# Optimization experiments

Hardware: AMD Instinct MI355X
Metric: run time of the kernel (lower is better)

Reference implementation:

```python
import jax, jax.numpy as jnp
import numpy as np

B, N, D, H = 8, 1024, 768, 12
DH = D // H
SCALE = D ** (-0.5)  # standard_scale=False => dim**-0.5


def setup_inputs() -> dict:
    key = jax.random.key(0)
    ks = jax.random.split(key, 6)
    x = jax.random.normal(ks[0], (B, N, D), dtype=jnp.float32)
    gamma = jax.random.uniform(ks[1], (B,), dtype=jnp.float32)
    dist = jax.random.uniform(ks[2], (N, N), dtype=jnp.float32)
    W_qkv = jax.random.normal(ks[3], (D, 3 * D), dtype=jnp.float32) * (D ** -0.5)
    b_qkv = jnp.zeros((3 * D,), dtype=jnp.float32)
    W_proj = jax.random.normal(ks[4], (D, D), dtype=jnp.float32) * (D ** -0.5)
    b_proj = jnp.zeros((D,), dtype=jnp.float32)
    return {"x": x, "gamma": gamma, "dist": dist, "W_qkv": W_qkv,
            "b_qkv": b_qkv, "W_proj": W_proj, "b_proj": b_proj}


def reference(x, gamma, dist, W_qkv, b_qkv, W_proj, b_proj):
    # qkv projection: [B,N,3D] -> [3,B,H,N,DH]
    qkv = (x @ W_qkv + b_qkv).reshape(B, N, 3, H, DH).transpose(2, 0, 3, 1, 4)
    q, k, v = qkv[0], qkv[1], qkv[2]
    # scores [B,H,N,N] with learned per-batch distance bias
    scores = jnp.einsum('bhnd,bhmd->bhnm', q, k) * SCALE
    scores = scores - gamma[:, None, None, None] * dist[None, None, :, :]
    attn = jax.nn.softmax(scores, axis=-1)
    out = jnp.einsum('bhnm,bhmd->bhnd', attn, v)
    out = out.transpose(0, 2, 1, 3).reshape(B, N, D)  # [B,N,D]
    return out @ W_proj + b_proj
```

## Files before the change

### kernel.cpp

```cpp
#include <hip/hip_runtime.h>
#include <hip/hip_bf16.h>
#include <cstdint>
#include <cstddef>

#define B_  8
#define N_  1024
#define D_  768
#define H_  12
#define DH_ 64
#define M_  (B_*N_)
#define D3_ (3*D_)

typedef __bf16 bf16;
typedef __bf16 bf16x4 __attribute__((ext_vector_type(4)));
typedef __bf16 bf16x8 __attribute__((ext_vector_type(8)));
typedef float  floatx4 __attribute__((ext_vector_type(4)));

__device__ __forceinline__ void async16(const void* g, void* l) {
  __builtin_amdgcn_global_load_lds(
      (const __attribute__((address_space(1))) unsigned int*)g,
      (__attribute__((address_space(3))) unsigned int*)l, 16, 0, 0);
}

__global__ __launch_bounds__(256) void detect_small_k(
    const unsigned int* __restrict__ xraw, const void* bq, const void* bp,
    const void* gm, int* __restrict__ flag, bf16* bqd, bf16* bpd, float* gmd) {
  __shared__ int sc;
  if (threadIdx.x == 0) sc = 0;
  __syncthreads();
  int cnt = 0;
  for (int j = 0; j < 8; j++) {
    unsigned int w = xraw[threadIdx.x * 8 + j];
    unsigned int e = (w >> 7) & 0xFF;
    cnt += (e >= 100 && e <= 140) ? 1 : 0;
  }
  atomicAdd(&sc, cnt);
  __syncthreads();
  int f = (sc > 1024) ? 1 : 0;
  if (threadIdx.x == 0) *flag = f;
  for (int i = threadIdx.x; i < D3_; i += 256)
    bqd[i] = f ? ((const bf16*)bq)[i] : (bf16)((const float*)bq)[i];
  for (int i = threadIdx.x; i < D_; i += 256)
    bpd[i] = f ? ((const bf16*)bp)[i] : (bf16)((const float*)bp)[i];
  if (threadIdx.x < B_)
    gmd[threadIdx.x] = f ? (float)((const bf16*)gm)[threadIdx.x]
                         : ((const float*)gm)[threadIdx.x];
}

__device__ __forceinline__ void ingest_span(const void* src, bf16* dst, int f,
                                            long n4, long i0, long stride) {
  if (f) {
    const ushort2* s = (const ushort2*)src;
    ushort2* d = (ushort2*)dst;
    for (long i = i0; i < n4 * 2; i += stride) d[i] = s[i];
  } else {
    const float4* s = (const float4*)src;
    for (long i = i0; i < n4; i += stride) {
      float4 v = s[i];
      bf16x4 o = { (bf16)v.x, (bf16)v.y, (bf16)v.z, (bf16)v.w };
      *(bf16x4*)(dst + i * 4) = o;
    }
  }
}
#define XBLOCKS 1024
#define DBLOCKS 256
__global__ __launch_bounds__(256) void ingest2_k(const void* __restrict__ x,
                                                 bf16* __restrict__ xb,
                                                 const void* __restrict__ dist,
                                                 bf16* __restrict__ distb,
                                                 const int* __restrict__ flag) {
  int f = *flag;
  if (blockIdx.x < XBLOCKS) {
    long i0 = (long)blockIdx.x * 256 + threadIdx.x;
    ingest_span(x, xb, f, (long)M_ * D_ / 4, i0, (long)XBLOCKS * 256);
  } else {
    long i0 = (long)(blockIdx.x - XBLOCKS) * 256 + threadIdx.x;
    ingest_span(dist, distb, f, (long)N_ * N_ / 4, i0, (long)DBLOCKS * 256);
  }
}

__global__ __launch_bounds__(256) void ingest_wt_k(const void* srcA, bf16* dstA,
                                                   const void* srcB, bf16* dstB,
                                                   const int* __restrict__ flag,
                                                   int tilesA, int tcA) {
  __shared__ bf16 t[64][72];
  int f = *flag;
  int bid = blockIdx.x;
  const void* src; bf16* dst; int C;
  int tc;
  if (bid < tilesA) { src = srcA; dst = dstA; C = D3_; tc = tcA; }
  else { bid -= tilesA; src = srcB; dst = dstB; C = D_; tc = D_ / 64; }
  int c0 = (bid % tc) * 64, r0 = (bid / tc) * 64;
  int i = threadIdx.x >> 2, j0 = (threadIdx.x & 3) * 16;
  if (f) {
    const bf16* s = (const bf16*)src + (size_t)(r0 + i) * C + c0 + j0;
#pragma unroll
    for (int jj = 0; jj < 16; jj += 8) *(bf16x8*)&t[i][j0 + jj] = *(const bf16x8*)(s + jj);
  } else {
    const float4* s = (const float4*)((const float*)src + (size_t)(r0 + i) * C + c0 + j0);
#pragma unroll
    for (int jj = 0; jj < 4; jj++) {
      float4 v = s[jj];
      bf16x4 o = { (bf16)v.x, (bf16)v.y, (bf16)v.z, (bf16)v.w };
      *(bf16x4*)&t[i][j0 + jj * 4] = o;
    }
  }
  __syncthreads();
  bf16* d = dst + (size_t)(c0 + i) * D_ + r0 + j0;
#pragma unroll
  for (int jj = 0; jj < 16; jj++) d[jj] = t[j0 + jj][i];
}

template <int MODE, int TMI, int BYL>
__global__ __launch_bounds__(256) void gemm_bt(const bf16* __restrict__ A,
                                               const bf16* __restrict__ Bt,
                                               const bf16* __restrict__ bias,
                                               bf16* __restrict__ O0,
                                               bf16* __restrict__ O1,
                                               bf16* __restrict__ O2,
                                               float* __restrict__ OF,
                                               const int* __restrict__ flag,
                                               int Kdim) {
  constexpr int TM = TMI * 32;
  constexpr int ASZ = 2 * TM * 32;
  int id = blockIdx.x;
  int xcd = id & 7;
  int j = id >> 3;
  int bx = j / BYL;
  int by = xcd * BYL + (j % BYL);
  int n0 = bx * 128, m0 = by * TM;
  int tid = threadIdx.x, wave = tid >> 6, lane = tid & 63;
  int wm = (wave >> 1) * (TMI * 16), wn = (wave & 1) * 64;
  int cl = lane & 15, qd = lane >> 4;
  __shared__ __align__(16) bf16 sh[ASZ + 2 * 128 * 32];
  floatx4 acc[TMI][4] = {};

  int srow = lane >> 2, sko = (lane & 3) * 8;

  auto stage = [&](int kt, int b) {
#pragma unroll
    for (int i = 0; i < TMI / 2; i++) {
      int c = wave * (TMI / 2) + i;
      int row = c * 16 + srow;
      async16(A + (size_t)(m0 + row) * Kdim + kt + sko,
              (char*)sh + (size_t)b * (TM * 64) + c * 1024);
    }
#pragma unroll
    for (int i = 0; i < 2; i++) {
      int c = wave * 2 + i;
      int row = c * 16 + srow;
      async16(Bt + (size_t)(n0 + row) * Kdim + kt + sko,
              (char*)sh + (size_t)ASZ * 2 + (size_t)b * 8192 + c * 1024);
    }
  };
  auto compute = [&](int b) {
    const bf16* Ab = sh + (size_t)b * (TM * 32);
    const bf16* Bb = sh + ASZ + (size_t)b * (128 * 32);
    bf16x8 af[TMI], bfv[4];
#pragma unroll
    for (int mi = 0; mi < TMI; mi++)
      af[mi] = *(const bf16x8*)(Ab + (wm + mi * 16 + cl) * 32 + qd * 8);
#pragma unroll
    for (int ni = 0; ni < 4; ni++)
      bfv[ni] = *(const bf16x8*)(Bb + (wn + ni * 16 + cl) * 32 + qd * 8);
#pragma unroll
    for (int mi = 0; mi < TMI; mi++)
#pragma unroll
      for (int ni = 0; ni < 4; ni++)
        acc[mi][ni] = __builtin_amdgcn_mfma_f32_16x16x32_bf16(af[mi], bfv[ni],
                                                              acc[mi][ni], 0, 0, 0);
  };

  stage(0, 0);
  for (int kt = 0; kt < Kdim; kt += 64) {
    __syncthreads();
    if (kt + 32 < Kdim) stage(kt + 32, 1);
    compute(0);
    __syncthreads();
    if (kt + 64 < Kdim) stage(kt + 64, 0);
    if (kt + 32 < Kdim) compute(1);
  }

  if constexpr (MODE == 0) {
    int t = n0 / D_;
    int h0 = (n0 % D_) >> 6;
    int b = m0 >> 10;
    int nbase = m0 & 1023;
    bf16* Ot = (t == 0) ? O0 : O1;
    __syncthreads();
#pragma unroll
    for (int hh = 0; hh < 2; hh++) {
      if ((wave >> 1) == hh) {
#pragma unroll
        for (int ni = 0; ni < 4; ni++) {
          int col = wn + ni * 16 + cl;
          float bv = (float)bias[n0 + col];
          int s = (col >> 3) & 7;
#pragma unroll
          for (int mi = 0; mi < TMI; mi++) {
            int qpos = (mi * 4 + qd) ^ s;
            bf16x4 w = { (bf16)(acc[mi][ni][0] + bv), (bf16)(acc[mi][ni][1] + bv),
                         (bf16)(acc[mi][ni][2] + bv), (bf16)(acc[mi][ni][3] + bv) };
            *(bf16x4*)((char*)sh + col * 144 + qpos * 8) = w;
          }
        }
      }
      __syncthreads();
      if (t < 2) {
#pragma unroll
        for (int it = 0; it < 4; it++) {
          int flat = it * 256 + tid;
          int rh = flat >> 3, jl = flat & 7;
          int hs = rh >> 6, rl = rh & 63;
          int cb = hs * 64 + jl * 8;
          int s = (cb >> 3) & 7;
          int q = rl >> 2, rr = rl & 3;
          bf16x8 w;
#pragma unroll
          for (int jj = 0; jj < 8; jj++)
            w[jj] = *(const bf16*)((char*)sh + (cb + jj) * 144 + ((q ^ s) * 8) + rr * 2);
          int ng = nbase + hh * 64 + rl;
          *(bf16x8*)(Ot + (((size_t)(b * H_ + h0 + hs) * N_ + ng) * DH_ + jl * 8)) = w;
        }
      } else {
#pragma unroll
        for (int it = 0; it < 4; it++) {
          int flat = it * 256 + tid;
          int col = flat >> 3, jl = flat & 7;
          int hs = col >> 6, d = col & 63;
          int s = (col >> 3) & 7;
          bf16x4 a0 = *(const bf16x4*)((char*)sh + col * 144 + (((2 * jl) ^ s) * 8));
          bf16x4 a1 = *(const bf16x4*)((char*)sh + col * 144 + (((2 * jl + 1) ^ s) * 8));
          bf16x8 w = { a0[0], a0[1], a0[2], a0[3], a1[0], a1[1], a1[2], a1[3] };
          int ng0 = nbase + hh * 64 + jl * 8;
          *(bf16x8*)(O2 + (((size_t)(b * H_ + h0 + hs) * DH_ + d) * N_ + ng0)) = w;
        }
      }
      __syncthreads();
    }
  } else {
    int fbf16 = *flag;
#pragma unroll
    for (int ni = 0; ni < 4; ni++) {
      int colb = n0 + wn + ni * 16;
      float bv = (float)bias[colb + cl];
#pragma unroll
      for (int mi = 0; mi < TMI; mi++) {
#pragma unroll
        for (int r = 0; r < 4; r++) {
          int row = m0 + wm + mi * 16 + qd * 4 + r;
          float v = acc[mi][ni][r] + bv;
          size_t oi = (size_t)row * D_ + colb + cl;
          if (fbf16) O0[oi] = (bf16)v;
          else       OF[oi] = v;
        }
      }
    }
  }
}

#define KROW 72
#define VROW 136
#define PSTR 136
__global__ __launch_bounds__(256, 4) void attn_k(const bf16* __restrict__ Q,
                                                 const bf16* __restrict__ Kp,
                                                 const bf16* __restrict__ Vt,
                                                 const float* __restrict__ gammaf,
                                                 const bf16* __restrict__ dist,
                                                 bf16* __restrict__ O) {
  int bh = blockIdx.x % (B_ * H_);
  int q0 = (blockIdx.x / (B_ * H_)) * 64;
  int b = bh / H_, h = bh % H_;
  int tid = threadIdx.x, wave = tid >> 6, lane = tid & 63;
  int cl = lane & 15, qd = lane >> 4;
  __shared__ __align__(16) bf16 Ks[128 * KROW];
  __shared__ __align__(16) bf16 Vs[64 * VROW];

  bf16x8 aq[2];
  {
    const bf16* Qg = Q + ((size_t)bh * N_ + q0 + wave * 16 + cl) * DH_;
    aq[0] = *(const bf16x8*)(Qg + qd * 8);
    aq[1] = *(const bf16x8*)(Qg + 32 + qd * 8);
  }

  floatx4 oacc[4] = {};
  float lsum = 0.f;
  const float LOG2E = 1.4426950408889634f;
  const float SCL = 0.03608439182435161f * LOG2E;
  float gl = gammaf[b] * LOG2E;

  const bf16* Kg0 = Kp + (size_t)bh * N_ * DH_;
  const bf16* Vg0 = Vt + (size_t)bh * DH_ * N_;
  const bf16* Dg  = dist + (size_t)(q0 + wave * 16 + cl) * N_ + qd * 4;
  int krow = tid >> 1, kh = tid & 1;
  int vrow = tid >> 2, vq = tid & 3;
  bf16* pslab = Ks + wave * 2304;

  for (int t0 = 0; t0 < N_; t0 += 128) {
    const bf16* Kg = Kg0 + (size_t)(t0 + krow) * DH_ + kh * 32;
    bf16x8 kv[4];
#pragma unroll
    for (int j = 0; j < 4; j++) kv[j] = *(const bf16x8*)(Kg + j * 8);
    const bf16* Vg = Vg0 + (size_t)vrow * N_ + t0 + vq * 8;
    bf16x8 vv[4];
#pragma unroll
    for (int p = 0; p < 4; p++) vv[p] = *(const bf16x8*)(Vg + p * 32);
    bf16x4 ddr[8];
#pragma unroll
    for (int ni = 0; ni < 8; ni++) ddr[ni] = *(const bf16x4*)(Dg + t0 + ni * 16);

    __syncthreads();
#pragma unroll
    for (int j = 0; j < 4; j++)
      *(bf16x8*)(Ks + krow * KROW + kh * 32 + j * 8) = kv[j];
#pragma unroll
    for (int p = 0; p < 4; p++)
      *(bf16x8*)(Vs + vrow * VROW + vq * 8 + p * 32) = vv[p];
    __syncthreads();

    floatx4 sacc[8] = {};
#pragma unroll
    for (int kk = 0; kk < 2; kk++) {
#pragma unroll
      for (int ni = 0; ni < 8; ni++) {
        bf16x8 ak = *(const bf16x8*)(Ks + (ni * 16 + cl) * KROW + kk * 32 + qd * 8);
        sacc[ni] = __builtin_amdgcn_mfma_f32_16x16x32_bf16(ak, aq[kk], sacc[ni], 0, 0, 0);
      }
    }

    bf16x4 pk[8];
#pragma unroll
    for (int ni = 0; ni < 8; ni++) {
#pragma unroll
      for (int r = 0; r < 4; r++) {
        float p = __builtin_exp2f(sacc[ni][r] * SCL - gl * (float)ddr[ni][r]);
        lsum += p;
        pk[ni][r] = (bf16)p;
      }
    }
    __syncthreads();

#pragma unroll
    for (int ni = 0; ni < 8; ni++)
      *(bf16x4*)(pslab + cl * PSTR + ni * 16 + qd * 4) = pk[ni];

#pragma unroll
    for (int kk = 0; kk < 4; kk++) {
      bf16x8 ap = *(const bf16x8*)(pslab + cl * PSTR + kk * 32 + qd * 8);
#pragma unroll
      for (int ni = 0; ni < 4; ni++) {
        bf16x8 bv = *(const bf16x8*)(Vs + (ni * 16 + cl) * VROW + kk * 32 + qd * 8);
        oacc[ni] = __builtin_amdgcn_mfma_f32_16x16x32_bf16(ap, bv, oacc[ni], 0, 0, 0);
      }
    }
  }

  lsum += __shfl_xor(lsum, 16, 64);
  lsum += __shfl_xor(lsum, 32, 64);

#pragma unroll
  for (int r = 0; r < 4; r++) {
    float inv = 1.f / __shfl(lsum, qd * 4 + r, 64);
    int qg = q0 + wave * 16 + qd * 4 + r;
    size_t base = ((size_t)(b * N_ + qg)) * D_ + h * DH_;
#pragma unroll
    for (int ni = 0; ni < 4; ni++)
      O[base + ni * 16 + cl] = (bf16)(oacc[ni][r] * inv);
  }
}

extern "C" void kernel_launch(void* const* d_in, const int* in_sizes, int n_in,
                              void* d_out, int out_size, void* d_ws, size_t ws_size,
                              hipStream_t stream) {
  const void* x     = d_in[0];
  const void* gamma = d_in[1];
  const void* dist  = d_in[2];
  const void* Wqkv  = d_in[3];
  const void* bqkv  = d_in[4];
  const void* Wproj = d_in[5];
  const void* bproj = d_in[6];

  char* ws = (char*)d_ws;
  size_t o = 0;
  int*   flag   = (int*)(ws + o);   o += 16;
  float* gammaf = (float*)(ws + o); o += 32;
  bf16*  xb     = (bf16*)(ws + o);  o += (size_t)M_ * D_ * 2;
  bf16*  distb  = (bf16*)(ws + o);  o += (size_t)N_ * N_ * 2;
  bf16*  bqkvb  = (bf16*)(ws + o);  o += (size_t)D3_ * 2;
  bf16*  bprojb = (bf16*)(ws + o);  o += (size_t)D_ * 2 + 8;
  bf16*  WqkvT  = (bf16*)(ws + o);  o += (size_t)D3_ * D_ * 2;
  bf16*  WprojT = (bf16*)(ws + o);  o += (size_t)D_ * D_ * 2;
  bf16*  Qp     = (bf16*)(ws + o);  o += (size_t)M_ * D_ * 2;
  bf16*  Kp     = (bf16*)(ws + o);  o += (size_t)M_ * D_ * 2;
  bf16*  Vtp    = (bf16*)(ws + o);  o += (size_t)M_ * D_ * 2;
  bf16*  Op     = (bf16*)(ws + o);  o += (size_t)M_ * D_ * 2;
  if (ws_size < o) return;

  detect_small_k<<<1, 256, 0, stream>>>((const unsigned int*)x, bqkv, bproj, gamma,
                                        flag, bqkvb, bprojb, gammaf);
  ingest2_k<<<XBLOCKS + DBLOCKS, 256, 0, stream>>>(x, xb, dist, distb, flag);
  int tilesA = (D3_ / 64) * (D_ / 64);
  int tilesB = (D_ / 64) * (D_ / 64);
  ingest_wt_k<<<tilesA + tilesB, 256, 0, stream>>>(Wqkv, WqkvT, Wproj, WprojT,
                                                   flag, tilesA, D3_ / 64);

  gemm_bt<0, 4, 8><<<18 * 64, 256, 0, stream>>>(
      xb, WqkvT, bqkvb, Qp, Kp, Vtp, nullptr, flag, D_);
  attn_k<<<dim3(B_ * H_ * (N_ / 64)), 256, 0, stream>>>(
      Qp, Kp, Vtp, gammaf, distb, Op);
  gemm_bt<1, 2, 16><<<6 * 128, 256, 0, stream>>>(
      Op, WprojT, bprojb, (bf16*)d_out, nullptr, nullptr, (float*)d_out, flag, D_);
}
```

Baseline: 268.9 us.

## Rewrite attention with 32x32 MFMA tiles, register-resident P and swizzled LDS

The attention kernel now processes 128 queries per block (32 per wave) with 32x32x16 bf16 MFMAs in place of 16x16x32. The probability tile is packed into registers with cvt_pk and permlane32_swap instead of making a round trip through LDS. K and V tiles are stored in XOR-swizzled LDS without padding, and the softmax scale times log2e is folded into Q in the QKV GEMM epilogue. The aim is fewer LDS accesses and barriers per tile and better MFMA efficiency, at the cost of higher register use (occupancy hint lowered to 3) and half as many blocks.

```diff
diff --git a/kernel.cpp b/kernel.cpp
--- a/kernel.cpp
+++ b/kernel.cpp
@@ -15,6 +15,8 @@
 typedef __bf16 bf16x4 __attribute__((ext_vector_type(4)));
 typedef __bf16 bf16x8 __attribute__((ext_vector_type(8)));
 typedef float  floatx4 __attribute__((ext_vector_type(4)));
+typedef float  floatx16 __attribute__((ext_vector_type(16)));
+typedef unsigned int uint32x4 __attribute__((ext_vector_type(4)));
 
 __device__ __forceinline__ void async16(const void* g, void* l) {
   __builtin_amdgcn_global_load_lds(
@@ -187,6 +189,7 @@
     int b = m0 >> 10;
     int nbase = m0 & 1023;
     bf16* Ot = (t == 0) ? O0 : O1;
+    float qs = (t == 0) ? (0.03608439182435161f * 1.4426950408889634f) : 1.f;
     __syncthreads();
 #pragma unroll
     for (int hh = 0; hh < 2; hh++) {
@@ -199,8 +202,10 @@
 #pragma unroll
           for (int mi = 0; mi < TMI; mi++) {
             int qpos = (mi * 4 + qd) ^ s;
-            bf16x4 w = { (bf16)(acc[mi][ni][0] + bv), (bf16)(acc[mi][ni][1] + bv),
-                         (bf16)(acc[mi][ni][2] + bv), (bf16)(acc[mi][ni][3] + bv) };
+            bf16x4 w = { (bf16)((acc[mi][ni][0] + bv) * qs),
+                         (bf16)((acc[mi][ni][1] + bv) * qs),
+                         (bf16)((acc[mi][ni][2] + bv) * qs),
+                         (bf16)((acc[mi][ni][3] + bv) * qs) };
             *(bf16x4*)((char*)sh + col * 144 + qpos * 8) = w;
           }
         }
@@ -259,113 +264,133 @@
   }
 }
 
-#define KROW 72
-#define VROW 136
-#define PSTR 136
-__global__ __launch_bounds__(256, 4) void attn_k(const bf16* __restrict__ Q,
+__global__ __launch_bounds__(256, 3) void attn_k(const bf16* __restrict__ Q,
                                                  const bf16* __restrict__ Kp,
                                                  const bf16* __restrict__ Vt,
                                                  const float* __restrict__ gammaf,
                                                  const bf16* __restrict__ dist,
                                                  bf16* __restrict__ O) {
   int bh = blockIdx.x % (B_ * H_);
-  int q0 = (blockIdx.x / (B_ * H_)) * 64;
+  int q0 = (blockIdx.x / (B_ * H_)) * 128;
   int b = bh / H_, h = bh % H_;
   int tid = threadIdx.x, wave = tid >> 6, lane = tid & 63;
-  int cl = lane & 15, qd = lane >> 4;
-  __shared__ __align__(16) bf16 Ks[128 * KROW];
-  __shared__ __align__(16) bf16 Vs[64 * VROW];
-
-  bf16x8 aq[2];
+  int l5 = lane & 31, hh = lane >> 5, l7 = lane & 7;
+  __shared__ __align__(16) bf16 Ks[128 * 64];
+  __shared__ __align__(16) bf16 Vs[64 * 128];
+  __shared__ float Ls[4 * 32];
+
+  bf16x8 aq[4];
   {
-    const bf16* Qg = Q + ((size_t)bh * N_ + q0 + wave * 16 + cl) * DH_;
-    aq[0] = *(const bf16x8*)(Qg + qd * 8);
-    aq[1] = *(const bf16x8*)(Qg + 32 + qd * 8);
-  }
-
-  floatx4 oacc[4] = {};
+    const bf16* Qg = Q + ((size_t)bh * N_ + q0 + wave * 32 + l5) * DH_ + hh * 8;
+#pragma unroll
+    for (int st = 0; st < 4; st++) aq[st] = *(const bf16x8*)(Qg + st * 16);
+  }
+
+  floatx16 oacc[2] = {};
   float lsum = 0.f;
   const float LOG2E = 1.4426950408889634f;
-  const float SCL = 0.03608439182435161f * LOG2E;
   float gl = gammaf[b] * LOG2E;
 
   const bf16* Kg0 = Kp + (size_t)bh * N_ * DH_;
   const bf16* Vg0 = Vt + (size_t)bh * DH_ * N_;
-  const bf16* Dg  = dist + (size_t)(q0 + wave * 16 + cl) * N_ + qd * 4;
-  int krow = tid >> 1, kh = tid & 1;
-  int vrow = tid >> 2, vq = tid & 3;
-  bf16* pslab = Ks + wave * 2304;
+  const bf16* Dg  = dist + (size_t)(q0 + wave * 32 + l5) * N_ + hh * 4;
+
+  int kofs[4], vofs[4];
+  const bf16* kg[4]; const bf16* vg[4];
+#pragma unroll
+  for (int i = 0; i < 4; i++) {
+    int id = tid + i * 256;
+    int kr = id >> 3, ksl = id & 7;
+    kofs[i] = kr * 128 + ((ksl ^ (kr & 7)) * 16);
+    kg[i] = Kg0 + (size_t)kr * DH_ + ksl * 8;
+    int vr = id >> 4, vsl = id & 15;
+    vofs[i] = vr * 256 + ((vsl ^ (vr & 7)) * 16);
+    vg[i] = Vg0 + (size_t)vr * N_ + vsl * 8;
+  }
+  int krd = l5 * 128;
+  int vrd = l5 * 256;
 
   for (int t0 = 0; t0 < N_; t0 += 128) {
-    const bf16* Kg = Kg0 + (size_t)(t0 + krow) * DH_ + kh * 32;
-    bf16x8 kv[4];
-#pragma unroll
-    for (int j = 0; j < 4; j++) kv[j] = *(const bf16x8*)(Kg + j * 8);
-    const bf16* Vg = Vg0 + (size_t)vrow * N_ + t0 + vq * 8;
-    bf16x8 vv[4];
-#pragma unroll
-    for (int p = 0; p < 4; p++) vv[p] = *(const bf16x8*)(Vg + p * 32);
-    bf16x4 ddr[8];
-#pragma unroll
-    for (int ni = 0; ni < 8; ni++) ddr[ni] = *(const bf16x4*)(Dg + t0 + ni * 16);
+    bf16x8 kv[4], vv[4];
+#pragma unroll
+    for (int i = 0; i < 4; i++) kv[i] = *(const bf16x8*)(kg[i] + (size_t)t0 * DH_);
+#pragma unroll
+    for (int i = 0; i < 4; i++) vv[i] = *(const bf16x8*)(vg[i] + t0);
+    bf16x4 ddr[16];
+#pragma unroll
+    for (int sub = 0; sub < 4; sub++)
+#pragma unroll
+      for (int jj = 0; jj < 4; jj++)
+        ddr[sub * 4 + jj] = *(const bf16x4*)(Dg + t0 + sub * 32 + jj * 8);
 
     __syncthreads();
 #pragma unroll
-    for (int j = 0; j < 4; j++)
-      *(bf16x8*)(Ks + krow * KROW + kh * 32 + j * 8) = kv[j];
-#pragma unroll
-    for (int p = 0; p < 4; p++)
-      *(bf16x8*)(Vs + vrow * VROW + vq * 8 + p * 32) = vv[p];
+    for (int i = 0; i < 4; i++) *(bf16x8*)((char*)Ks + kofs[i]) = kv[i];
+#pragma unroll
+    for (int i = 0; i < 4; i++) *(bf16x8*)((char*)Vs + vofs[i]) = vv[i];
     __syncthreads();
 
-    floatx4 sacc[8] = {};
-#pragma unroll
-    for (int kk = 0; kk < 2; kk++) {
-#pragma unroll
-      for (int ni = 0; ni < 8; ni++) {
-        bf16x8 ak = *(const bf16x8*)(Ks + (ni * 16 + cl) * KROW + kk * 32 + qd * 8);
-        sacc[ni] = __builtin_amdgcn_mfma_f32_16x16x32_bf16(ak, aq[kk], sacc[ni], 0, 0, 0);
-      }
-    }
-
-    bf16x4 pk[8];
-#pragma unroll
-    for (int ni = 0; ni < 8; ni++) {
-#pragma unroll
-      for (int r = 0; r < 4; r++) {
-        float p = __builtin_exp2f(sacc[ni][r] * SCL - gl * (float)ddr[ni][r]);
-        lsum += p;
-        pk[ni][r] = (bf16)p;
-      }
-    }
-    __syncthreads();
-
-#pragma unroll
-    for (int ni = 0; ni < 8; ni++)
-      *(bf16x4*)(pslab + cl * PSTR + ni * 16 + qd * 4) = pk[ni];
-
-#pragma unroll
-    for (int kk = 0; kk < 4; kk++) {
-      bf16x8 ap = *(const bf16x8*)(pslab + cl * PSTR + kk * 32 + qd * 8);
-#pragma unroll
-      for (int ni = 0; ni < 4; ni++) {
-        bf16x8 bv = *(const bf16x8*)(Vs + (ni * 16 + cl) * VROW + kk * 32 + qd * 8);
-        oacc[ni] = __builtin_amdgcn_mfma_f32_16x16x32_bf16(ap, bv, oacc[ni], 0, 0, 0);
-      }
-    }
-  }
-
-  lsum += __shfl_xor(lsum, 16, 64);
+#pragma unroll
+    for (int sub = 0; sub < 4; sub++) {
+      floatx16 s = {};
+      __builtin_amdgcn_s_setprio(1);
+#pragma unroll
+      for (int st = 0; st < 4; st++) {
+        bf16x8 ak = *(const bf16x8*)((char*)Ks + sub * 4096 + krd +
+                                     (((st * 2 + hh) ^ l7) * 16));
+        s = __builtin_amdgcn_mfma_f32_32x32x16_bf16(ak, aq[st], s, 0, 0, 0);
+      }
+      __builtin_amdgcn_s_setprio(0);
+
+      float p[16];
+#pragma unroll
+      for (int r = 0; r < 16; r++) {
+        float df = (float)ddr[sub * 4 + (r >> 2)][r & 3];
+        p[r] = __builtin_exp2f(__builtin_fmaf(-gl, df, s[r]));
+        lsum += p[r];
+      }
+      unsigned pw[8];
+#pragma unroll
+      for (int i = 0; i < 8; i++) {
+        unsigned o_;
+        asm("v_cvt_pk_bf16_f32 %0, %1, %2"
+            : "=v"(o_) : "v"(p[2 * i]), "v"(p[2 * i + 1]));
+        pw[i] = o_;
+      }
+      asm("v_permlane32_swap_b32 %0, %1" : "+v"(pw[0]), "+v"(pw[2]));
+      asm("v_permlane32_swap_b32 %0, %1" : "+v"(pw[1]), "+v"(pw[3]));
+      asm("v_permlane32_swap_b32 %0, %1" : "+v"(pw[4]), "+v"(pw[6]));
+      asm("v_permlane32_swap_b32 %0, %1" : "+v"(pw[5]), "+v"(pw[7]));
+      bf16x8 pa0, pa1;
+      { uint32x4 u0 = { pw[0], pw[1], pw[2], pw[3] }; pa0 = *(bf16x8*)&u0; }
+      { uint32x4 u1 = { pw[4], pw[5], pw[6], pw[7] }; pa1 = *(bf16x8*)&u1; }
+
+      __builtin_amdgcn_s_setprio(1);
+#pragma unroll
+      for (int t = 0; t < 2; t++) {
+        bf16x8 bv0 = *(const bf16x8*)((char*)Vs + t * 8192 + vrd +
+                                      (((sub * 4 + hh) ^ l7) * 16));
+        oacc[t] = __builtin_amdgcn_mfma_f32_32x32x16_bf16(pa0, bv0, oacc[t], 0, 0, 0);
+        bf16x8 bv1 = *(const bf16x8*)((char*)Vs + t * 8192 + vrd +
+                                      (((sub * 4 + 2 + hh) ^ l7) * 16));
+        oacc[t] = __builtin_amdgcn_mfma_f32_32x32x16_bf16(pa1, bv1, oacc[t], 0, 0, 0);
+      }
+      __builtin_amdgcn_s_setprio(0);
+    }
+  }
+
   lsum += __shfl_xor(lsum, 32, 64);
-
-#pragma unroll
-  for (int r = 0; r < 4; r++) {
-    float inv = 1.f / __shfl(lsum, qd * 4 + r, 64);
-    int qg = q0 + wave * 16 + qd * 4 + r;
-    size_t base = ((size_t)(b * N_ + qg)) * D_ + h * DH_;
-#pragma unroll
-    for (int ni = 0; ni < 4; ni++)
-      O[base + ni * 16 + cl] = (bf16)(oacc[ni][r] * inv);
+  float inv = 1.f / lsum;
+  Ls[wave * 32 + l5] = inv;
+  __syncthreads();
+  size_t obase = ((size_t)b * N_ + q0 + wave * 32) * D_ + h * DH_;
+#pragma unroll
+  for (int r = 0; r < 16; r++) {
+    int qrow = (r & 3) + 8 * (r >> 2) + 4 * hh;
+    float iv = Ls[wave * 32 + qrow];
+#pragma unroll
+    for (int t = 0; t < 2; t++)
+      O[obase + (size_t)qrow * D_ + t * 32 + l5] = (bf16)(oacc[t][r] * iv);
   }
 }
 
@@ -406,7 +431,7 @@
 
   gemm_bt<0, 4, 8><<<18 * 64, 256, 0, stream>>>(
       xb, WqkvT, bqkvb, Qp, Kp, Vtp, nullptr, flag, D_);
-  attn_k<<<dim3(B_ * H_ * (N_ / 64)), 256, 0, stream>>>(
+  attn_k<<<dim3(B_ * H_ * (N_ / 128)), 256, 0, stream>>>(
       Qp, Kp, Vtp, gammaf, distb, Op);
   gemm_bt<1, 2, 16><<<6 * 128, 256, 0, stream>>>(
       Op, WprojT, bprojb, (bf16*)d_out, nullptr, nullptr, (float*)d_out, flag, D_);
```

Result: faster. 261.2 us (-2.9%).
